# Performance work log

Measured on AMD Instinct MI355X. Metric: run time of the kernel, lower is better.

Reference implementation:

```python
import jax, jax.numpy as jnp
import numpy as np

IN_DIM = 1024
HID = 1024
DEPTH = 13            # perfect binary tree: 2**13 = 8192 leaves, 8191 internal nodes
N_LEAVES = 2 ** DEPTH
N_TOKENS = 8192
N_OPS = 4             # '+', '/', '*', '-' (ordered_op=False)


def setup_inputs() -> dict:
    key = jax.random.key(0)
    ks = jax.random.split(key, 16)
    sW = 1.0 / np.sqrt(IN_DIM)
    sU = 1.0 / np.sqrt(HID)
    inp = {
        "tokens": jax.random.normal(ks[0], (N_TOKENS, IN_DIM), jnp.float32),
        "leaf_token_ids": jax.random.randint(ks[1], (N_LEAVES,), 0, N_TOKENS),
        "op_ids": jax.random.randint(ks[2], (N_LEAVES - 1,), 0, N_OPS),
        "W_i": jax.random.normal(ks[3], (HID, IN_DIM), jnp.float32) * sW,
        "W_o": jax.random.normal(ks[4], (HID, IN_DIM), jnp.float32) * sW,
        "W_u": jax.random.normal(ks[5], (HID, IN_DIM), jnp.float32) * sW,
        "W_f": jax.random.normal(ks[6], (HID, IN_DIM), jnp.float32) * sW,
        "U_i": jax.random.normal(ks[7], (HID, HID), jnp.float32) * sU,
        "U_o": jax.random.normal(ks[8], (HID, HID), jnp.float32) * sU,
        "U_u": jax.random.normal(ks[9], (HID, HID), jnp.float32) * sU,
        "U_f": jax.random.normal(ks[10], (HID, HID), jnp.float32) * sU,
        "b_i": jnp.zeros((1, HID), jnp.float32),
        "b_o": jnp.zeros((1, HID), jnp.float32),
        "b_u": jnp.zeros((1, HID), jnp.float32),
        "b_f": jnp.zeros((1, HID), jnp.float32),
        "op_emb": jax.random.uniform(ks[11], (N_OPS, IN_DIM), jnp.float32, -1.0, 1.0),
        "c_init": jnp.zeros((2, HID), jnp.float32),
        "h_init": jnp.zeros((2, HID), jnp.float32),
    }
    return inp


def reference(tokens, leaf_token_ids, op_ids, W_i, W_o, W_u, W_f,
              U_i, U_o, U_u, U_f, b_i, b_o, b_u, b_f,
              op_emb, c_init, h_init):
    """Depth-batched Child-Sum TreeLSTM over a perfect binary tree.
    op_ids are stored root-first level order: level l (root=0) occupies
    op_ids[2**l - 1 : 2**(l+1) - 1]. Leaves are level DEPTH.
    Children of node j at level l are nodes 2j, 2j+1 at level l+1.
    Returns jnp.stack([c_root, h_root])  -> [2, 1, HID]."""
    H = U_i.shape[0]

    def node_step(x, c_state, h_state):
        # x: [n, in_dim]; c_state/h_state: [n, 2, H]
        h_sum = h_state.sum(axis=1)                                   # [n, H]
        i = jax.nn.sigmoid(x @ W_i.T + h_sum @ U_i.T + b_i)
        o = jax.nn.sigmoid(x @ W_o.T + h_sum @ U_o.T + b_o)
        u = jnp.tanh(x @ W_u.T + h_sum @ U_u.T + b_u)
        f = jax.nn.sigmoid((x @ W_f.T)[:, None, :] + h_state @ U_f.T + b_f)  # [n,2,H]
        c = i * u + (f * c_state).sum(axis=1)                         # [n, H]
        h = o * jnp.tanh(c)
        return c, h

    n = leaf_token_ids.shape[0]
    depth = int(np.log2(n))
    # leaves: learnable init states, x = embedding of the token
    x = tokens[leaf_token_ids]                                        # [n, in_dim]
    c, h = node_step(x,
                     jnp.broadcast_to(c_init, (n, 2, H)),
                     jnp.broadcast_to(h_init, (n, 2, H)))
    # internal levels, bottom-up
    for l in range(depth - 1, -1, -1):
        m = 2 ** l
        off = m - 1
        x = op_emb[op_ids[off:off + m]]                               # [m, in_dim]
        c, h = node_step(x, c.reshape(m, 2, H), h.reshape(m, 2, H))
    return jnp.stack([c, h])  # [2, 1, H]: root (c, h)
```

## Files before the change

### kernel.cpp

```cpp
#include <hip/hip_runtime.h>

typedef unsigned short u16;
typedef __attribute__((ext_vector_type(4))) unsigned short us4;
typedef __attribute__((ext_vector_type(4))) float f4;
typedef __attribute__((ext_vector_type(8))) short bf16x8;
typedef __attribute__((ext_vector_type(4))) float f32x4;

__device__ __forceinline__ u16 f2bf(float x) {
  unsigned u = __float_as_uint(x);
  return (u16)((u + 0x7FFFu + ((u >> 16) & 1u)) >> 16);
}
__device__ __forceinline__ float b2f(u16 s) {
  return __uint_as_float(((unsigned)s) << 16);
}
__device__ __forceinline__ float sigm(float x) { return 1.f / (1.f + __expf(-x)); }
__device__ __forceinline__ float tanhf_(float x) { return 2.f / (1.f + __expf(-2.f * x)) - 1.f; }

__global__ void setup_kernel(
    const float* __restrict__ tokens, const int* __restrict__ leaf_ids,
    const float* __restrict__ w0, const float* __restrict__ w1,
    const float* __restrict__ w2, const float* __restrict__ w3,
    const float* __restrict__ u0, const float* __restrict__ u1,
    const float* __restrict__ u2, const float* __restrict__ u3,
    const float* __restrict__ b0, const float* __restrict__ b1,
    const float* __restrict__ b2, const float* __restrict__ b3,
    const float* __restrict__ op_emb, const float* __restrict__ h_init,
    u16* __restrict__ Wb, u16* __restrict__ Ub, u16* __restrict__ Xl,
    float* __restrict__ xw, float* __restrict__ leafC) {
  const int bid = blockIdx.x;
  if (bid < 8192) {
    int mat = bid >> 10;
    int off4 = (int)(bid & 1023) * 256 + threadIdx.x;
    const float* src; u16* dst;
    switch (mat) {
      case 0: src = w0; dst = Wb; break;
      case 1: src = w1; dst = Wb + 1048576; break;
      case 2: src = w2; dst = Wb + 2097152; break;
      case 3: src = w3; dst = Wb + 3145728; break;
      case 4: src = u0; dst = Ub; break;
      case 5: src = u1; dst = Ub + 1048576; break;
      case 6: src = u2; dst = Ub + 2097152; break;
      default: src = u3; dst = Ub + 3145728; break;
    }
    f4 v = ((const f4*)src)[off4];
    us4 o = {f2bf(v[0]), f2bf(v[1]), f2bf(v[2]), f2bf(v[3])};
    ((us4*)dst)[off4] = o;
  } else if (bid < 16384) {
    int n = bid - 8192, t = threadIdx.x;
    int tok = leaf_ids[n];
    f4 v = ((const f4*)(tokens + (size_t)tok * 1024))[t];
    us4 o = {f2bf(v[0]), f2bf(v[1]), f2bf(v[2]), f2bf(v[3])};
    ((us4*)(Xl + (size_t)n * 1024))[t] = o;
  } else {
    const int wave = threadIdx.x >> 6, lane = threadIdx.x & 63;
    const int wid = (bid - 16384) * 4 + wave;
    const f4* xr;
    const f4* wr;
    float bias;
    bool dual = false;
    const f4* xr2 = nullptr;
    float* dst;
    if (wid < 16384) {
      int op = wid >> 12, g = (wid >> 10) & 3, j = wid & 1023;
      const float* wsrc; const float* bs;
      switch (g) {
        case 0: wsrc = w0; bs = b0; break;
        case 1: wsrc = w1; bs = b1; break;
        case 2: wsrc = w2; bs = b2; break;
        default: wsrc = w3; bs = b3; break;
      }
      xr = (const f4*)(op_emb + (size_t)op * 1024);
      wr = (const f4*)(wsrc + (size_t)j * 1024);
      bias = bs[j];
      dst = xw + wid;
    } else {
      int id2 = wid - 16384;
      int sel = id2 >> 10, j = id2 & 1023;
      const f4* h0 = (const f4*)h_init;
      const f4* h1 = (const f4*)(h_init + 1024);
      if (sel < 3) {
        const float* usrc; const float* bs;
        switch (sel) {
          case 0: usrc = u0; bs = b0; break;
          case 1: usrc = u1; bs = b1; break;
          default: usrc = u2; bs = b2; break;
        }
        xr = h0; xr2 = h1; dual = true;
        wr = (const f4*)(usrc + (size_t)j * 1024);
        bias = bs[j];
      } else {
        xr = (sel == 3) ? h0 : h1;
        wr = (const f4*)(u3 + (size_t)j * 1024);
        bias = b3[j];
      }
      dst = leafC + id2;
    }
    float s = 0.f;
#pragma unroll
    for (int i = 0; i < 4; ++i) {
      int k = lane + 64 * i;
      f4 a = xr[k];
      if (dual) {
        f4 a2 = xr2[k];
        a[0] += a2[0]; a[1] += a2[1]; a[2] += a2[2]; a[3] += a2[3];
      }
      f4 b = wr[k];
      s += a[0] * b[0] + a[1] * b[1] + a[2] * b[2] + a[3] * b[3];
    }
#pragma unroll
    for (int off = 32; off > 0; off >>= 1) s += __shfl_xor(s, off);
    if (lane == 0) *dst = s + bias;
  }
}

template <int NRT, int NCT>
__global__ __launch_bounds__(256, (NRT == 8 ? 2 : 3)) void tree_gemm(
    const u16* __restrict__ A, const u16* __restrict__ Wm,
    const float* __restrict__ consts,
    const int* __restrict__ ops,
    const float* __restrict__ c_in,
    float* __restrict__ c_out, u16* __restrict__ h_out,
    int nrows, int m_parents, int is_leaf, float* __restrict__ out_root) {
  constexpr int ROWS = NRT * 16;
  constexpr int COLS = NCT * 16;
  constexpr int S = 64 / NCT;
  constexpr int LOG2S = (NCT == 2 ? 5 : 4);
  constexpr int NST = NRT / 2;
  constexpr int DBUF = NRT * 2048;
  constexpr int PASSES = (NRT == 8 ? 4 : (NRT == 4 ? 2 : 1));
  constexpr int RPP = ROWS / PASSES;
  constexpr int FPP = RPP / 16;
  constexpr int SMEM_U16 =
      (4 * RPP * 68 > NRT * 2048 ? 4 * RPP * 68 : NRT * 2048);
  __shared__ __align__(16) u16 smem[SMEM_U16];
  char* smem_c = (char*)smem;

  const int tid = threadIdx.x;
  const int wave = tid >> 6;
  const int lane = tid & 63;
  const int stripe = blockIdx.x & (S - 1);
  const int rowblk = blockIdx.x >> LOG2S;
  const int r0 = rowblk * ROWS;
  const int j0 = stripe * COLS;
  const int ln15 = lane & 15, quad = lane >> 4;
  const int sub = lane >> 3, gsel = lane & 7;

  const char* pAsrc[NST];
  unsigned a_dst[NST];
#pragma unroll
  for (int i = 0; i < NST; ++i) {
    int slot = (wave * NST + i) * 8 + sub;
    int row = r0 + slot; if (row >= nrows) row = nrows - 1;
    pAsrc[i] = (const char*)(A + (size_t)row * 1024 + (unsigned)((gsel ^ sub) * 8));
    a_dst[i] = (unsigned)((wave * NST + i) * 1024 + lane * 16);
  }
  const char* pB[NCT];
#pragma unroll
  for (int f = 0; f < NCT; ++f)
    pB[f] = (const char*)(Wm + (size_t)(wave * 1024 + j0 + f * 16 + ln15) * 1024 + quad * 8);

  unsigned a_base[2];
#pragma unroll
  for (int ks = 0; ks < 2; ++ks)
    a_base[ks] = (unsigned)(ln15 * 128 + (((ks * 4 + quad) ^ (ln15 & 7)) * 16));

  f32x4 acc[NRT][NCT];
#pragma unroll
  for (int t = 0; t < NRT; ++t)
#pragma unroll
    for (int f = 0; f < NCT; ++f) acc[t][f] = (f32x4){0.f, 0.f, 0.f, 0.f};

#pragma unroll
  for (int i = 0; i < NST; ++i)
    __builtin_amdgcn_global_load_lds(
        (const __attribute__((address_space(1))) void*)(pAsrc[i]),
        (__attribute__((address_space(3))) void*)(smem_c + a_dst[i]), 16, 0, 0);
  bf16x8 bcur[2][NCT], bnxt[2][NCT];
#pragma unroll
  for (int ks = 0; ks < 2; ++ks)
#pragma unroll
    for (int f = 0; f < NCT; ++f)
      bcur[ks][f] = *(const bf16x8*)(pB[f] + ks * 64);

#pragma unroll
  for (int ch = 0; ch < 16; ++ch) {
    __syncthreads();
    if (ch < 15) {
#pragma unroll
      for (int i = 0; i < NST; ++i)
        __builtin_amdgcn_global_load_lds(
            (const __attribute__((address_space(1))) void*)(pAsrc[i] + (ch + 1) * 128),
            (__attribute__((address_space(3))) void*)(smem_c + ((ch + 1) & 1) * DBUF + a_dst[i]),
            16, 0, 0);
    }
    const unsigned cb = (unsigned)((ch & 1) * DBUF);
    {
      bf16x8 af[NRT];
#pragma unroll
      for (int t = 0; t < NRT; ++t)
        af[t] = *(const bf16x8*)(smem_c + cb + a_base[0] + t * 2048);
#pragma unroll
      for (int t = 0; t < NRT; ++t)
#pragma unroll
        for (int f = 0; f < NCT; ++f)
          acc[t][f] = __builtin_amdgcn_mfma_f32_16x16x32_bf16(af[t], bcur[0][f],
                                                              acc[t][f], 0, 0, 0);
    }
    if (ch < 15) {
#pragma unroll
      for (int ks = 0; ks < 2; ++ks)
#pragma unroll
        for (int f = 0; f < NCT; ++f)
          bnxt[ks][f] = *(const bf16x8*)(pB[f] + (ch + 1) * 128 + ks * 64);
    }
    {
      bf16x8 af[NRT];
#pragma unroll
      for (int t = 0; t < NRT; ++t)
        af[t] = *(const bf16x8*)(smem_c + cb + a_base[1] + t * 2048);
#pragma unroll
      for (int t = 0; t < NRT; ++t)
#pragma unroll
        for (int f = 0; f < NCT; ++f)
          acc[t][f] = __builtin_amdgcn_mfma_f32_16x16x32_bf16(af[t], bcur[1][f],
                                                              acc[t][f], 0, 0, 0);
    }
#pragma unroll
    for (int ks = 0; ks < 2; ++ks)
#pragma unroll
      for (int f = 0; f < NCT; ++f) bcur[ks][f] = bnxt[ks][f];
  }

#pragma unroll
  for (int pass = 0; pass < PASSES; ++pass) {
    __syncthreads();
#pragma unroll
    for (int tt = 0; tt < FPP; ++tt) {
      int t = pass * FPP + tt;
#pragma unroll
      for (int f = 0; f < NCT; ++f)
#pragma unroll
        for (int k = 0; k < 4; ++k) {
          int row = tt * 16 + quad * 4 + k;
          int col = f * 16 + ln15;
          smem[(wave * RPP + row) * 68 + col] = f2bf(acc[t][f][k]);
        }
    }
    __syncthreads();
    const int rbase = r0 + pass * RPP;

    if (is_leaf) {
      for (int e = tid; e < RPP * COLS; e += 256) {
        int r = e / COLS, j = e % COLS;
        int col = j0 + j, n = rbase + r;
        float p0 = b2f(smem[(0 * RPP + r) * 68 + j]);
        float p1 = b2f(smem[(1 * RPP + r) * 68 + j]);
        float p2 = b2f(smem[(2 * RPP + r) * 68 + j]);
        float p3 = b2f(smem[(3 * RPP + r) * 68 + j]);
        float i_ = sigm(p0 + consts[col]);
        float o_ = sigm(p1 + consts[1024 + col]);
        float u_ = tanhf_(p2 + consts[2048 + col]);
        float f0 = sigm(p3 + consts[3072 + col]);
        float f1 = sigm(p3 + consts[4096 + col]);
        float c = i_ * u_ + f0 * c_in[col] + f1 * c_in[1024 + col];
        float h = o_ * tanhf_(c);
        c_out[(size_t)n * 1024 + col] = c;
        h_out[(size_t)n * 1024 + col] = f2bf(h);
      }
    } else {
      for (int e = tid; e < (RPP / 2) * COLS; e += 256) {
        int p = e / COLS, j = e % COLS;
        int np = (rbase >> 1) + p;
        if (np >= m_parents) break;
        int col = j0 + j;
        int op = ops[np];
        const float* xwop = consts + ((unsigned)(op * 4) << 10);
        float p0a = b2f(smem[(0 * RPP + 2 * p) * 68 + j]), p0b = b2f(smem[(0 * RPP + 2 * p + 1) * 68 + j]);
        float p1a = b2f(smem[(1 * RPP + 2 * p) * 68 + j]), p1b = b2f(smem[(1 * RPP + 2 * p + 1) * 68 + j]);
        float p2a = b2f(smem[(2 * RPP + 2 * p) * 68 + j]), p2b = b2f(smem[(2 * RPP + 2 * p + 1) * 68 + j]);
        float p3a = b2f(smem[(3 * RPP + 2 * p) * 68 + j]), p3b = b2f(smem[(3 * RPP + 2 * p + 1) * 68 + j]);
        float i_ = sigm(p0a + p0b + xwop[col]);
        float o_ = sigm(p1a + p1b + xwop[1024 + col]);
        float u_ = tanhf_(p2a + p2b + xwop[2048 + col]);
        float f0 = sigm(p3a + xwop[3072 + col]);
        float f1 = sigm(p3b + xwop[3072 + col]);
        float c = i_ * u_ + f0 * c_in[(size_t)(rbase + 2 * p) * 1024 + col]
                          + f1 * c_in[(size_t)(rbase + 2 * p + 1) * 1024 + col];
        float h = o_ * tanhf_(c);
        if (m_parents == 1) {
          out_root[col] = c;
          out_root[1024 + col] = h;
        } else {
          c_out[(size_t)np * 1024 + col] = c;
          h_out[(size_t)np * 1024 + col] = f2bf(h);
        }
      }
    }
  }
}

extern "C" void kernel_launch(void* const* d_in, const int* in_sizes, int n_in,
                              void* d_out, int out_size, void* d_ws, size_t ws_size,
                              hipStream_t stream) {
  const float* tokens = (const float*)d_in[0];
  const int* leaf_ids = (const int*)d_in[1];
  const int* op_ids = (const int*)d_in[2];
  const float* W0 = (const float*)d_in[3];
  const float* W1 = (const float*)d_in[4];
  const float* W2 = (const float*)d_in[5];
  const float* W3 = (const float*)d_in[6];
  const float* U0 = (const float*)d_in[7];
  const float* U1 = (const float*)d_in[8];
  const float* U2 = (const float*)d_in[9];
  const float* U3 = (const float*)d_in[10];
  const float* B0 = (const float*)d_in[11];
  const float* B1 = (const float*)d_in[12];
  const float* B2 = (const float*)d_in[13];
  const float* B3 = (const float*)d_in[14];
  const float* op_emb = (const float*)d_in[15];
  const float* c_init = (const float*)d_in[16];
  const float* h_init = (const float*)d_in[17];
  float* out = (float*)d_out;

  char* ws = (char*)d_ws;
  u16* Wb = (u16*)ws;
  u16* Ub = Wb + (size_t)4 * 1024 * 1024;
  u16* Xl = Ub + (size_t)4 * 1024 * 1024;
  u16* hA = Xl + (size_t)8192 * 1024;
  u16* hB = hA + (size_t)8192 * 1024;
  float* cA = (float*)(hB + (size_t)4096 * 1024);
  float* cB = cA + (size_t)8192 * 1024;
  float* xw = cB + (size_t)4096 * 1024;
  float* lc = xw + 16 * 1024;

  setup_kernel<<<21760, 256, 0, stream>>>(tokens, leaf_ids,
                                          W0, W1, W2, W3, U0, U1, U2, U3,
                                          B0, B1, B2, B3, op_emb, h_init,
                                          Wb, Ub, Xl, xw, lc);

  tree_gemm<8, 2><<<64 * 32, 256, 0, stream>>>(Xl, Wb, lc, nullptr, c_init,
                                               cA, hA, 8192, 0, 1, out);

  const u16* hin = hA; const float* cin = cA;
  u16* hout = hB; float* cout = cB;
  for (int l = 12; l >= 0; --l) {
    int m = 1 << l;
    int nrows = 2 * m;
    if (nrows >= 2048) {
      tree_gemm<8, 2><<<(nrows / 128) * 32, 256, 0, stream>>>(
          hin, Ub, xw, op_ids + (m - 1), cin, cout, hout, nrows, m, 0, out);
    } else if (nrows >= 1024) {
      tree_gemm<4, 2><<<(nrows / 64) * 32, 256, 0, stream>>>(
          hin, Ub, xw, op_ids + (m - 1), cin, cout, hout, nrows, m, 0, out);
    } else {
      int rg = nrows / 32; if (rg < 1) rg = 1;
      tree_gemm<2, 2><<<rg * 32, 256, 0, stream>>>(
          hin, Ub, xw, op_ids + (m - 1), cin, cout, hout, nrows, m, 0, out);
    }
    const u16* th = hin; hin = hout; hout = (u16*)th;
    const float* tc = cin; cin = cout; cout = (float*)tc;
  }
}
```

Baseline: 567.0 us.

## Add specialized small-level GEMM that streams U weights directly from global memory

Adds a dedicated kernel for the upper tree levels (fewer than 1024 rows). It loads the whole 32-row activation tile into LDS once with swizzled async global-to-LDS loads and reads the U weight fragments straight from global memory into registers, with no LDS staging. The intent is to cut per-launch latency and synchronisation for the small, latency-bound levels, where the generic tiled kernel spends most of its time in pipeline overhead. The catch is that the weight reads are uncoalesced-ish and go straight from global memory into registers, so the kernel may stall waiting on memory.

```diff
diff --git a/kernel.cpp b/kernel.cpp
--- a/kernel.cpp
+++ b/kernel.cpp
@@ -299,6 +299,112 @@
   }
 }
 
+__global__ __launch_bounds__(256, 2) void small_gemm(
+    const u16* __restrict__ A, const u16* __restrict__ Um,
+    const float* __restrict__ xw, const int* __restrict__ ops,
+    const float* __restrict__ c_in,
+    float* __restrict__ c_out, u16* __restrict__ h_out,
+    int nrows, int m_parents, float* __restrict__ out_root) {
+  __shared__ __align__(16) u16 smem[32768];
+  char* smem_c = (char*)smem;
+  const int tid = threadIdx.x;
+  const int wave = tid >> 6, lane = tid & 63;
+  const int stripe = blockIdx.x & 31, rowblk = blockIdx.x >> 5;
+  const int r0 = rowblk * 32, j0 = stripe * 32;
+  const int ln15 = lane & 15, quad = lane >> 4;
+  const int sub = lane >> 3, gsel = lane & 7;
+
+#pragma unroll
+  for (int i = 0; i < 16; ++i) {
+    int w = wave * 16 + i;
+    int ch = w >> 2;
+    int row = r0 + (w & 3) * 8 + sub;
+    if (row >= nrows) row = nrows - 1;
+    const char* src = (const char*)(A + (size_t)row * 1024 + (unsigned)(ch * 64) + (unsigned)((gsel ^ sub) * 8));
+    __builtin_amdgcn_global_load_lds(
+        (const __attribute__((address_space(1))) void*)src,
+        (__attribute__((address_space(3))) void*)(smem_c + w * 1024 + lane * 16), 16, 0, 0);
+  }
+  const char* pB[2];
+#pragma unroll
+  for (int f = 0; f < 2; ++f)
+    pB[f] = (const char*)(Um + (size_t)(wave * 1024 + j0 + f * 16 + ln15) * 1024 + quad * 8);
+  unsigned a_base[2];
+#pragma unroll
+  for (int ks = 0; ks < 2; ++ks)
+    a_base[ks] = (unsigned)(ln15 * 128 + (((ks * 4 + quad) ^ (ln15 & 7)) * 16));
+
+  f32x4 acc[2][2];
+#pragma unroll
+  for (int t = 0; t < 2; ++t)
+#pragma unroll
+    for (int f = 0; f < 2; ++f) acc[t][f] = (f32x4){0.f, 0.f, 0.f, 0.f};
+
+  __syncthreads();
+
+#pragma unroll
+  for (int ch = 0; ch < 16; ++ch) {
+    bf16x8 b[2][2];
+#pragma unroll
+    for (int ks = 0; ks < 2; ++ks)
+#pragma unroll
+      for (int f = 0; f < 2; ++f)
+        b[ks][f] = *(const bf16x8*)(pB[f] + ch * 128 + ks * 64);
+#pragma unroll
+    for (int ks = 0; ks < 2; ++ks) {
+      bf16x8 af[2];
+#pragma unroll
+      for (int t = 0; t < 2; ++t)
+        af[t] = *(const bf16x8*)(smem_c + ch * 4096 + a_base[ks] + t * 2048);
+#pragma unroll
+      for (int t = 0; t < 2; ++t)
+#pragma unroll
+        for (int f = 0; f < 2; ++f)
+          acc[t][f] = __builtin_amdgcn_mfma_f32_16x16x32_bf16(af[t], b[ks][f], acc[t][f], 0, 0, 0);
+    }
+  }
+
+  __syncthreads();
+#pragma unroll
+  for (int t = 0; t < 2; ++t)
+#pragma unroll
+    for (int f = 0; f < 2; ++f)
+#pragma unroll
+      for (int k = 0; k < 4; ++k) {
+        int row = t * 16 + quad * 4 + k;
+        int col = f * 16 + ln15;
+        smem[(wave * 32 + row) * 68 + col] = f2bf(acc[t][f][k]);
+      }
+  __syncthreads();
+  for (int e = tid; e < 16 * 32; e += 256) {
+    int p = e >> 5, j = e & 31;
+    int np = (r0 >> 1) + p;
+    if (np >= m_parents) break;
+    int col = j0 + j;
+    int op = ops[np];
+    const float* xwop = xw + ((unsigned)op << 12);
+    float p0a = b2f(smem[(0 * 32 + 2 * p) * 68 + j]), p0b = b2f(smem[(0 * 32 + 2 * p + 1) * 68 + j]);
+    float p1a = b2f(smem[(1 * 32 + 2 * p) * 68 + j]), p1b = b2f(smem[(1 * 32 + 2 * p + 1) * 68 + j]);
+    float p2a = b2f(smem[(2 * 32 + 2 * p) * 68 + j]), p2b = b2f(smem[(2 * 32 + 2 * p + 1) * 68 + j]);
+    float p3a = b2f(smem[(3 * 32 + 2 * p) * 68 + j]), p3b = b2f(smem[(3 * 32 + 2 * p + 1) * 68 + j]);
+    float i_ = sigm(p0a + p0b + xwop[col]);
+    float o_ = sigm(p1a + p1b + xwop[1024 + col]);
+    float u_ = tanhf_(p2a + p2b + xwop[2048 + col]);
+    float f0 = sigm(p3a + xwop[3072 + col]);
+    float f1 = sigm(p3b + xwop[3072 + col]);
+    float c = i_ * u_ + f0 * c_in[(size_t)(r0 + 2 * p) * 1024 + col]
+                      + f1 * c_in[(size_t)(r0 + 2 * p + 1) * 1024 + col];
+    float h = o_ * tanhf_(c);
+    if (m_parents == 1) {
+      out_root[col] = c;
+      out_root[1024 + col] = h;
+    } else {
+      c_out[(size_t)np * 1024 + col] = c;
+      h_out[(size_t)np * 1024 + col] = f2bf(h);
+    }
+  }
+}
+
 extern "C" void kernel_launch(void* const* d_in, const int* in_sizes, int n_in,
                               void* d_out, int out_size, void* d_ws, size_t ws_size,
                               hipStream_t stream) {
@@ -354,8 +460,8 @@
           hin, Ub, xw, op_ids + (m - 1), cin, cout, hout, nrows, m, 0, out);
     } else {
       int rg = nrows / 32; if (rg < 1) rg = 1;
-      tree_gemm<2, 2><<<rg * 32, 256, 0, stream>>>(
-          hin, Ub, xw, op_ids + (m - 1), cin, cout, hout, nrows, m, 0, out);
+      small_gemm<<<rg * 32, 256, 0, stream>>>(
+          hin, Ub, xw, op_ids + (m - 1), cin, cout, hout, nrows, m, out);
     }
     const u16* th = hin; hin = hout; hout = (u16*)th;
     const float* tc = cin; cin = cout; cout = (float*)tc;
```

New measurement: 551.1 us. 1.03x faster.
